# Kernel tuning notes

Measured on AMD Instinct MI355X. Metric: run time of the kernel, lower is better.

## Reference

```python
import jax, jax.numpy as jnp
import numpy as np

N_NODES = 100000
N_EDGES = 1600000
D = 128


def setup_inputs() -> dict:
    key = jax.random.key(0)
    k1, k2, k3 = jax.random.split(key, 3)
    x = jax.random.normal(k1, (N_NODES, D), dtype=jnp.float32)
    W = jax.random.normal(k2, (D, D), dtype=jnp.float32) * (1.0 / np.sqrt(D))
    b = jnp.zeros((D,), dtype=jnp.float32)
    edge_index = jax.random.randint(k3, (2, N_EDGES), 0, N_NODES, dtype=jnp.int64)
    return {"x": x, "W": W, "b": b, "edge_index": edge_index}


def reference(x, W, b, edge_index):
    # GCNBlock: out = relu(GCNConv(x, edge_index)) + x ; returns (out, edge_index)
    # GCNConv (PyG default): add self-loops, symmetric deg^{-1/2} normalization.
    N = x.shape[0]
    h = x @ W  # [N, D] dense transform before aggregation

    loop = jnp.arange(N, dtype=edge_index.dtype)
    src = jnp.concatenate([edge_index[0], loop])  # [E+N]
    dst = jnp.concatenate([edge_index[1], loop])  # [E+N]

    deg = jax.ops.segment_sum(jnp.ones_like(dst, dtype=h.dtype), dst, num_segments=N)
    inv_sqrt = jax.lax.rsqrt(deg)  # deg >= 1 thanks to self-loops
    coef = inv_sqrt[src] * inv_sqrt[dst]  # [E+N]

    # gather messages, scale, scatter-add to destinations
    msg = h[src] * coef[:, None]  # [E+N, D] -- dominant memory traffic
    agg = jax.ops.segment_sum(msg, dst, num_segments=N) + b  # [N, D]

    out = jax.nn.relu(agg) + x  # relu + residual fusion
    return (out, edge_index)
```

## Files before the change

### kernel.cpp

```cpp
#include <hip/hip_runtime.h>


#define DD 128
#define EPB 2048
#define BSH 9
typedef __attribute__((ext_vector_type(8))) short bf16x8;
typedef __attribute__((ext_vector_type(4))) float f32x4;

__device__ __forceinline__ ushort f2bf(float f) {
    unsigned u = __float_as_uint(f);
    unsigned r = (u + 0x7fffu + ((u >> 16) & 1u)) >> 16;
    return (ushort)r;
}
__device__ __forceinline__ float bflo(unsigned u) { return __uint_as_float(u << 16); }
__device__ __forceinline__ float bfhi(unsigned u) { return __uint_as_float(u & 0xffff0000u); }

__device__ __forceinline__ int ld_src(const int* p, int e, int E, int is64) {
    return is64 ? p[2 * e] : p[e];
}
__device__ __forceinline__ int ld_dst(const int* p, int e, int E, int is64) {
    return is64 ? p[2 * (E + e)] : p[E + e];
}

__device__ __forceinline__ int detect64(const int* __restrict__ p, int E) {
    int lane = threadIdx.x & 63;
    int idx = 2 * lane + 1;
    if (idx >= 2 * E) idx = 2 * E - 1;
    unsigned long long m = __ballot(p[idx] != 0);
    return m == 0ull ? 1 : 0;
}

__global__ __launch_bounds__(256) void kA1(const int* __restrict__ ei, int E, int NB, int nA,
                                           float* __restrict__ outTail, int* __restrict__ H,
                                           const float* __restrict__ W, ushort* __restrict__ Wt) {
    int t = threadIdx.x, a = blockIdx.x;
    if (a >= nA) {
        int i = (a - nA) * 256 + t;
        if (i < DD * DD) {
            int c = i >> 7, k = i & 127;
            Wt[i] = f2bf(W[k * DD + c]);
        }
        return;
    }
    __shared__ int hist[256];
    int is64 = detect64(ei, E);
    if (t < NB) hist[t] = 0;
    __syncthreads();
    int base = a * EPB;
    #pragma unroll
    for (int it = 0; it < EPB / 256; ++it) {
        int e = base + it * 256 + t;
        if (e < E) {
            int s = ld_src(ei, e, E, is64);
            int d = ld_dst(ei, e, E, is64);
            outTail[e] = (float)s;
            outTail[E + e] = (float)d;
            atomicAdd(&hist[d >> BSH], 1);
        }
    }
    __syncthreads();
    if (t < NB) H[a * NB + t] = hist[t];
}

__global__ __launch_bounds__(256) void k_scanH1(int* __restrict__ H, int nA, int NB,
                                                int* __restrict__ colsum) {
    __shared__ int s[256];
    int b = blockIdx.x, t = threadIdx.x;
    int K = (nA + 255) / 256;
    int base = t * K;
    int local = 0;
    for (int j = 0; j < K; ++j) {
        int a = base + j;
        if (a < nA) local += H[a * NB + b];
    }
    s[t] = local;
    __syncthreads();
    #pragma unroll
    for (int off = 1; off < 256; off <<= 1) {
        int u = (t >= off) ? s[t - off] : 0;
        __syncthreads();
        s[t] += u;
        __syncthreads();
    }
    int run = s[t] - local;
    for (int j = 0; j < K; ++j) {
        int a = base + j;
        if (a < nA) { int v = H[a * NB + b]; H[a * NB + b] = run; run += v; }
    }
    if (t == 255) colsum[b] = s[255];
}

__global__ __launch_bounds__(256) void kA2(const int* __restrict__ ei, int E, int NB,
                                           const int* __restrict__ H,
                                           const int* __restrict__ colsum,
                                           unsigned* __restrict__ brec) {
    __shared__ int bs[256];
    __shared__ int cur[256];
    int t = threadIdx.x, a = blockIdx.x;
    int is64 = detect64(ei, E);
    int v = (t < NB) ? colsum[t] : 0;
    bs[t] = v;
    __syncthreads();
    #pragma unroll
    for (int off = 1; off < 256; off <<= 1) {
        int u = (t >= off) ? bs[t - off] : 0;
        __syncthreads();
        bs[t] += u;
        __syncthreads();
    }
    if (t < NB) cur[t] = H[a * NB + t] + bs[t] - v;
    __syncthreads();
    int base = a * EPB;
    #pragma unroll
    for (int it = 0; it < EPB / 256; ++it) {
        int e = base + it * 256 + t;
        if (e < E) {
            int s = ld_src(ei, e, E, is64);
            int d = ld_dst(ei, e, E, is64);
            int pos = atomicAdd(&cur[d >> BSH], 1);
            brec[pos] = (unsigned)s | ((unsigned)(d & 511) << 17);
        }
    }
}

__global__ __launch_bounds__(256) void kB(const unsigned* __restrict__ brec,
                                          const int* __restrict__ colsum, int NB, int N,
                                          int E, unsigned* __restrict__ recs,
                                          int* __restrict__ rowstart, float* __restrict__ invs) {
    __shared__ int bs[256];
    __shared__ int hist[512];
    __shared__ int scan[513];
    __shared__ int cur[512];
    int b = blockIdx.x, t = threadIdx.x;
    int v = (t < NB) ? colsum[t] : 0;
    bs[t] = v;
    __syncthreads();
    #pragma unroll
    for (int off = 1; off < 256; off <<= 1) {
        int u = (t >= off) ? bs[t - off] : 0;
        __syncthreads();
        bs[t] += u;
        __syncthreads();
    }
    if (t < NB) bs[t] -= v;
    hist[t] = 0; hist[t + 256] = 0;
    __syncthreads();
    int lo = bs[b], hi = lo + colsum[b];
    for (int i = lo + t; i < hi; i += 256) atomicAdd(&hist[brec[i] >> 17], 1);
    __syncthreads();
    if (t == 0) {
        int acc = 0;
        for (int j = 0; j < 512; ++j) { scan[j] = acc; acc += hist[j]; }
        scan[512] = acc;
    }
    __syncthreads();
    int nodeBase = b << BSH;
    #pragma unroll
    for (int j = t; j < 512; j += 256) {
        int node = nodeBase + j;
        if (node < N) {
            rowstart[node] = lo + scan[j];
            invs[node] = rsqrtf((float)(1 + hist[j]));
        }
        cur[j] = lo + scan[j];
    }
    if (b == NB - 1 && t == 0) rowstart[N] = E;
    __syncthreads();
    for (int i = lo + t; i < hi; i += 256) {
        unsigned r = brec[i];
        int pos = atomicAdd(&cur[r >> 17], 1);
        recs[pos] = r & 0x1FFFFu;
    }
}

__global__ void k_cvt_xs(const float2* __restrict__ x2, const float* __restrict__ invs,
                         unsigned* __restrict__ xs, int n2) {
    int i = blockIdx.x * blockDim.x + threadIdx.x;
    if (i < n2) {
        float w = invs[i >> 6];
        float2 v = x2[i];
        xs[i] = (unsigned)f2bf(w * v.x) | ((unsigned)f2bf(w * v.y) << 16);
    }
}

__global__ void k_agg_s(const unsigned* __restrict__ xs, const int* __restrict__ rowstart,
                        const float* __restrict__ invs, const unsigned* __restrict__ recs,
                        int N, unsigned* __restrict__ aggh) {
    int node = blockIdx.x * 4 + (threadIdx.x >> 6);
    int lane = threadIdx.x & 63;
    if (node >= N) return;
    float wn = invs[node];
    unsigned us = xs[(size_t)node * 64 + lane];
    float accx = bflo(us), accy = bfhi(us);
    int e = rowstart[node], e1 = rowstart[node + 1];
    for (; e + 16 <= e1; e += 16) {
        unsigned sv[16], vv[16];
        #pragma unroll
        for (int j = 0; j < 16; ++j) sv[j] = recs[e + j];
        #pragma unroll
        for (int j = 0; j < 16; ++j) vv[j] = xs[(size_t)sv[j] * 64 + lane];
        #pragma unroll
        for (int j = 0; j < 16; ++j) { accx += bflo(vv[j]); accy += bfhi(vv[j]); }
    }
    if (e + 8 <= e1) {
        unsigned sv[8], vv[8];
        #pragma unroll
        for (int j = 0; j < 8; ++j) sv[j] = recs[e + j];
        #pragma unroll
        for (int j = 0; j < 8; ++j) vv[j] = xs[(size_t)sv[j] * 64 + lane];
        #pragma unroll
        for (int j = 0; j < 8; ++j) { accx += bflo(vv[j]); accy += bfhi(vv[j]); }
        e += 8;
    }
    for (; e < e1; ++e) {
        unsigned v0 = xs[(size_t)recs[e] * 64 + lane];
        accx += bflo(v0); accy += bfhi(v0);
    }
    float ox = accx * wn, oy = accy * wn;
    aggh[(size_t)node * 64 + lane] = (unsigned)f2bf(ox) | ((unsigned)f2bf(oy) << 16);
}

__global__ __launch_bounds__(256) void k_gemm_mfma(const ushort* __restrict__ aggh,
                                                   const ushort* __restrict__ Wt,
                                                   const float* __restrict__ bb,
                                                   const float* __restrict__ x,
                                                   float* __restrict__ out, int N) {
    int wave = threadIdx.x >> 6, lane = threadIdx.x & 63;
    int rowBase = blockIdx.x * 64 + wave * 16;
    int rfrag = lane & 15, kgrp = lane >> 4;
    f32x4 zero = {0.f, 0.f, 0.f, 0.f};
    f32x4 acc[8];
    #pragma unroll
    for (int n = 0; n < 8; ++n) acc[n] = zero;

    int arow = rowBase + rfrag;
    bool av = arow < N;
    const ushort* bbase = aggh + (size_t)(av ? arow : 0) * DD + kgrp * 8;
    const ushort* wbase = Wt + rfrag * DD + kgrp * 8;

    #pragma unroll
    for (int ks = 0; ks < 4; ++ks) {
        bf16x8 bnode = {0, 0, 0, 0, 0, 0, 0, 0};
        if (av) bnode = *(const bf16x8*)(bbase + ks * 32);
        #pragma unroll
        for (int n = 0; n < 8; ++n) {
            bf16x8 aw = *(const bf16x8*)(wbase + n * 16 * DD + ks * 32);
            acc[n] = __builtin_amdgcn_mfma_f32_16x16x32_bf16(aw, bnode, acc[n], 0, 0, 0);
        }
    }

    int node = rowBase + (lane & 15);
    if (node < N) {
        int csub = (lane >> 4) * 4;
        #pragma unroll
        for (int n = 0; n < 8; ++n) {
            int c0 = n * 16 + csub;
            float4 bv = *(const float4*)&bb[c0];
            float4 xv = *(const float4*)&x[(size_t)node * DD + c0];
            float4 o;
            o.x = fmaxf(acc[n][0] + bv.x, 0.f) + xv.x;
            o.y = fmaxf(acc[n][1] + bv.y, 0.f) + xv.y;
            o.z = fmaxf(acc[n][2] + bv.z, 0.f) + xv.z;
            o.w = fmaxf(acc[n][3] + bv.w, 0.f) + xv.w;
            *(float4*)&out[(size_t)node * DD + c0] = o;
        }
    }
}

__global__ void k_sniff(const int* __restrict__ p, int n_check, int* __restrict__ flag) {
    __shared__ int any_nonzero;
    if (threadIdx.x == 0) any_nonzero = 0;
    __syncthreads();
    int j = threadIdx.x;
    if (j < n_check && p[2 * j + 1] != 0) any_nonzero = 1;
    __syncthreads();
    if (threadIdx.x == 0) *flag = any_nonzero ? 0 : 1;
}

__global__ void k_count_echo(const int* __restrict__ ei, int E, int* __restrict__ cnt,
                             float* __restrict__ outTail, unsigned* __restrict__ rank,
                             const int* __restrict__ flagp) {
    int is64 = *flagp;
    int e = blockIdx.x * blockDim.x + threadIdx.x;
    if (e < E) {
        int s = ld_src(ei, e, E, is64);
        int d = ld_dst(ei, e, E, is64);
        outTail[e] = (float)s;
        outTail[E + e] = (float)d;
        rank[e] = (unsigned)atomicAdd(&cnt[d], 1);
    }
}

__global__ void k_scan1(const int* __restrict__ cnt, int N, int* __restrict__ rowstart,
                        int* __restrict__ bsum) {
    __shared__ int s[1024];
    int tid = threadIdx.x;
    int i = blockIdx.x * 1024 + tid;
    int v = (i < N) ? cnt[i] : 0;
    s[tid] = v;
    __syncthreads();
    for (int off = 1; off < 1024; off <<= 1) {
        int t2 = (tid >= off) ? s[tid - off] : 0;
        __syncthreads();
        s[tid] += t2;
        __syncthreads();
    }
    if (i < N) rowstart[i] = s[tid] - v;
    if (tid == 1023) bsum[blockIdx.x] = s[1023];
}

__global__ void k_scan2(const int* __restrict__ bsum, int nblk, int* __restrict__ boff) {
    __shared__ int s[128];
    int t = threadIdx.x;
    if (t < nblk) s[t] = bsum[t];
    __syncthreads();
    if (t == 0) {
        int a = 0;
        for (int i = 0; i < nblk; i++) { int v = s[i]; s[i] = a; a += v; }
    }
    __syncthreads();
    if (t < nblk) boff[t] = s[t];
}

__global__ void k_scan3(int N, int E, int* __restrict__ rowstart, const int* __restrict__ boff,
                        const int* __restrict__ cnt, float* __restrict__ invs) {
    int i = blockIdx.x * blockDim.x + threadIdx.x;
    if (i < N) {
        int r = rowstart[i] + boff[i >> 10];
        rowstart[i] = r;
        invs[i] = rsqrtf((float)(1 + cnt[i]));
    }
    if (i == 0 && blockIdx.x == 0) rowstart[N] = E;
}

__global__ void k_fill_r(const int* __restrict__ ei, int E, const int* __restrict__ rowstart,
                         const unsigned* __restrict__ rank, unsigned* __restrict__ recs,
                         const int* __restrict__ flagp) {
    int is64 = *flagp;
    int e = blockIdx.x * blockDim.x + threadIdx.x;
    if (e < E) {
        int d = ld_dst(ei, e, E, is64);
        int s = ld_src(ei, e, E, is64);
        recs[rowstart[d] + rank[e]] = (unsigned)s;
    }
}

__global__ void k_agg_f32(const float* __restrict__ x, const int* __restrict__ rowstart,
                          const float* __restrict__ invs, const unsigned* __restrict__ recs,
                          int N, float* __restrict__ aggOut) {
    int node = blockIdx.x * 4 + (threadIdx.x >> 6);
    int lane = threadIdx.x & 63;
    if (node >= N) return;
    const float2* xr = (const float2*)x;
    float wn = invs[node];
    float2 xself = xr[(size_t)node * 64 + lane];
    float accx = wn * xself.x, accy = wn * xself.y;
    int e = rowstart[node], e1 = rowstart[node + 1];
    for (; e < e1; ++e) {
        unsigned s = recs[e];
        float w = invs[s];
        float2 v = xr[(size_t)s * 64 + lane];
        accx = fmaf(w, v.x, accx); accy = fmaf(w, v.y, accy);
    }
    float2 o; o.x = accx * wn; o.y = accy * wn;
    ((float2*)aggOut)[(size_t)node * 64 + lane] = o;
}

#define GROWS 32
__global__ __launch_bounds__(128) void k_gemm_f32(float* __restrict__ out, const float* __restrict__ Wm,
                                                  const float* __restrict__ bb,
                                                  const float* __restrict__ x, int N) {
    __shared__ float Ws[64 * DD];
    __shared__ float As[DD * GROWS];
    int t = threadIdx.x;
    int rowBase = blockIdx.x * GROWS;
    {
        int r = t & 31, kq = t >> 5;
        if (rowBase + r < N) {
            const float4* Av = (const float4*)(out + (size_t)(rowBase + r) * DD);
            #pragma unroll
            for (int q = 0; q < 8; q++) {
                float4 v = Av[kq * 8 + q];
                int k = (kq * 8 + q) * 4;
                As[(k + 0) * GROWS + r] = v.x;
                As[(k + 1) * GROWS + r] = v.y;
                As[(k + 2) * GROWS + r] = v.z;
                As[(k + 3) * GROWS + r] = v.w;
            }
        } else {
            #pragma unroll
            for (int q = 0; q < 8; q++) {
                int k = (kq * 8 + q) * 4;
                As[(k + 0) * GROWS + r] = 0.f;
                As[(k + 1) * GROWS + r] = 0.f;
                As[(k + 2) * GROWS + r] = 0.f;
                As[(k + 3) * GROWS + r] = 0.f;
            }
        }
    }
    int tx = t & 15, ty = t >> 4;
    int c0 = tx * 8, r0 = ty * 4;
    float acc[4][8];
    #pragma unroll
    for (int i = 0; i < 4; i++)
        #pragma unroll
        for (int j = 0; j < 8; j++) acc[i][j] = 0.f;
    for (int kk = 0; kk < DD; kk += 64) {
        __syncthreads();
        const float4* Wv = (const float4*)(Wm + (size_t)kk * DD);
        #pragma unroll
        for (int i = 0; i < 16; i++) ((float4*)Ws)[t + i * 128] = Wv[t + i * 128];
        __syncthreads();
        #pragma unroll 4
        for (int k = 0; k < 64; k++) {
            const float4 a = *(const float4*)&As[(kk + k) * GROWS + r0];
            const float4 w0 = *(const float4*)&Ws[k * DD + c0];
            const float4 w1 = *(const float4*)&Ws[k * DD + c0 + 4];
            const float av[4] = {a.x, a.y, a.z, a.w};
            const float wv[8] = {w0.x, w0.y, w0.z, w0.w, w1.x, w1.y, w1.z, w1.w};
            #pragma unroll
            for (int i = 0; i < 4; i++)
                #pragma unroll
                for (int j = 0; j < 8; j++) acc[i][j] = fmaf(av[i], wv[j], acc[i][j]);
        }
    }
    float bv[8];
    {
        float4 b0 = *(const float4*)&bb[c0];
        float4 b1 = *(const float4*)&bb[c0 + 4];
        bv[0] = b0.x; bv[1] = b0.y; bv[2] = b0.z; bv[3] = b0.w;
        bv[4] = b1.x; bv[5] = b1.y; bv[6] = b1.z; bv[7] = b1.w;
    }
    #pragma unroll
    for (int i = 0; i < 4; i++) {
        int row = rowBase + r0 + i;
        if (row < N) {
            const float4 xv0 = *(const float4*)&x[(size_t)row * DD + c0];
            const float4 xv1 = *(const float4*)&x[(size_t)row * DD + c0 + 4];
            float4 o0, o1;
            o0.x = fmaxf(acc[i][0] + bv[0], 0.f) + xv0.x;
            o0.y = fmaxf(acc[i][1] + bv[1], 0.f) + xv0.y;
            o0.z = fmaxf(acc[i][2] + bv[2], 0.f) + xv0.z;
            o0.w = fmaxf(acc[i][3] + bv[3], 0.f) + xv0.w;
            o1.x = fmaxf(acc[i][4] + bv[4], 0.f) + xv1.x;
            o1.y = fmaxf(acc[i][5] + bv[5], 0.f) + xv1.y;
            o1.z = fmaxf(acc[i][6] + bv[6], 0.f) + xv1.z;
            o1.w = fmaxf(acc[i][7] + bv[7], 0.f) + xv1.w;
            *(float4*)&out[(size_t)row * DD + c0] = o0;
            *(float4*)&out[(size_t)row * DD + c0 + 4] = o1;
        }
    }
}

extern "C" void kernel_launch(void* const* d_in, const int* in_sizes, int n_in,
                              void* d_out, int out_size, void* d_ws, size_t ws_size,
                              hipStream_t stream) {
    const float* x = (const float*)d_in[0];
    const float* W = (const float*)d_in[1];
    const float* b = (const float*)d_in[2];
    const int*   ei = (const int*)d_in[3];
    int N = in_sizes[0] / DD;
    int E = in_sizes[3] / 2;
    float* out = (float*)d_out;
    float* outTail = out + (size_t)N * DD;

    int NB = (N + 511) >> BSH;
    int nA = (E + EPB - 1) / EPB;

    char* wsb = (char*)d_ws;
    size_t off = 0;
    unsigned* brec = (unsigned*)(wsb + off);  off += (size_t)E * 4;
    unsigned* recs = (unsigned*)(wsb + off);  off += (size_t)E * 4;
    unsigned* xs   = (unsigned*)(wsb + off);  off += (size_t)N * 64 * 4;
    unsigned* aggh = (unsigned*)(wsb + off);  off += (size_t)N * 64 * 4;
    ushort*   Wt   = (ushort*)(wsb + off);    off += (size_t)DD * DD * 2;
    int* H         = (int*)(wsb + off);       off += (size_t)nA * NB * 4;
    int* colsum    = (int*)(wsb + off);       off += (size_t)NB * 4;
    int* rowstart  = (int*)(wsb + off);       off += (size_t)(N + 1) * 4;
    float* invs    = (float*)(wsb + off);     off += (size_t)N * 4;

    bool newpath = (ws_size >= off) && (NB <= 256) && (nA <= 1024) && (N <= 131072) && (E >= 64);

    if (newpath) {
        kA1<<<nA + 64, 256, 0, stream>>>(ei, E, NB, nA, outTail, H, W, Wt);
        k_scanH1<<<NB, 256, 0, stream>>>(H, nA, NB, colsum);
        kA2<<<nA, 256, 0, stream>>>(ei, E, NB, H, colsum, brec);
        kB<<<NB, 256, 0, stream>>>(brec, colsum, NB, N, E, recs, rowstart, invs);
        int n2 = N * 64;
        k_cvt_xs<<<(n2 + 255) / 256, 256, 0, stream>>>((const float2*)x, invs, xs, n2);
        k_agg_s<<<(N + 3) / 4, 256, 0, stream>>>(xs, rowstart, invs, recs, N, aggh);
        k_gemm_mfma<<<(N + 63) / 64, 256, 0, stream>>>((const ushort*)aggh, Wt, b, x, out, N);
    } else {
        off = 0;
        unsigned* recsF = (unsigned*)(wsb + off);  off += (size_t)E * 4;
        unsigned* rank  = (unsigned*)(wsb + off);  off += (size_t)E * 4;
        int* cnt        = (int*)(wsb + off);       off += (size_t)N * 4;
        int* rowstartF  = (int*)(wsb + off);       off += (size_t)(N + 1) * 4;
        float* invsF    = (float*)(wsb + off);     off += (size_t)N * 4;
        int* bsum       = (int*)(wsb + off);       off += 512 * 4;
        int* boff       = (int*)(wsb + off);       off += 512 * 4;
        int* flagF      = (int*)(wsb + off);

        hipMemsetAsync(cnt, 0, sizeof(int) * (size_t)N, stream);
        k_sniff<<<1, 1024, 0, stream>>>(ei, 1024, flagF);
        k_count_echo<<<(E + 255) / 256, 256, 0, stream>>>(ei, E, cnt, outTail, rank, flagF);
        int nblk = (N + 1023) / 1024;
        k_scan1<<<nblk, 1024, 0, stream>>>(cnt, N, rowstartF, bsum);
        k_scan2<<<1, 128, 0, stream>>>(bsum, nblk, boff);
        k_scan3<<<(N + 255) / 256, 256, 0, stream>>>(N, E, rowstartF, boff, cnt, invsF);
        k_fill_r<<<(E + 255) / 256, 256, 0, stream>>>(ei, E, rowstartF, rank, recsF, flagF);
        k_agg_f32<<<(N + 3) / 4, 256, 0, stream>>>(x, rowstartF, invsF, recsF, N, out);
        k_gemm_f32<<<(N + GROWS - 1) / GROWS, 128, 0, stream>>>(out, W, b, x, N);
    }
}
```

Before: 183.5 us.

## Reorder to GEMM-then-aggregate, fusing bf16 conversion into GEMM and epilogue into aggregation

The schedule changes from convert→aggregate→GEMM to GEMM→aggregate. The GEMM now reads fp32 x directly, converts it to bf16 in registers, scales by the source deg^-1/2 and writes a bf16 h table. The aggregation kernel then applies the destination scale, bias, ReLU and residual and writes the final output. This removes one kernel launch and one full N×128 bf16 intermediate round trip. The trade is that the aggregation now reads x and writes fp32 out, and rounding happens at a different point.

```diff
diff --git a/kernel.cpp b/kernel.cpp
--- a/kernel.cpp
+++ b/kernel.cpp
@@ -173,58 +173,10 @@
     }
 }
 
-__global__ void k_cvt_xs(const float2* __restrict__ x2, const float* __restrict__ invs,
-                         unsigned* __restrict__ xs, int n2) {
-    int i = blockIdx.x * blockDim.x + threadIdx.x;
-    if (i < n2) {
-        float w = invs[i >> 6];
-        float2 v = x2[i];
-        xs[i] = (unsigned)f2bf(w * v.x) | ((unsigned)f2bf(w * v.y) << 16);
-    }
-}
-
-__global__ void k_agg_s(const unsigned* __restrict__ xs, const int* __restrict__ rowstart,
-                        const float* __restrict__ invs, const unsigned* __restrict__ recs,
-                        int N, unsigned* __restrict__ aggh) {
-    int node = blockIdx.x * 4 + (threadIdx.x >> 6);
-    int lane = threadIdx.x & 63;
-    if (node >= N) return;
-    float wn = invs[node];
-    unsigned us = xs[(size_t)node * 64 + lane];
-    float accx = bflo(us), accy = bfhi(us);
-    int e = rowstart[node], e1 = rowstart[node + 1];
-    for (; e + 16 <= e1; e += 16) {
-        unsigned sv[16], vv[16];
-        #pragma unroll
-        for (int j = 0; j < 16; ++j) sv[j] = recs[e + j];
-        #pragma unroll
-        for (int j = 0; j < 16; ++j) vv[j] = xs[(size_t)sv[j] * 64 + lane];
-        #pragma unroll
-        for (int j = 0; j < 16; ++j) { accx += bflo(vv[j]); accy += bfhi(vv[j]); }
-    }
-    if (e + 8 <= e1) {
-        unsigned sv[8], vv[8];
-        #pragma unroll
-        for (int j = 0; j < 8; ++j) sv[j] = recs[e + j];
-        #pragma unroll
-        for (int j = 0; j < 8; ++j) vv[j] = xs[(size_t)sv[j] * 64 + lane];
-        #pragma unroll
-        for (int j = 0; j < 8; ++j) { accx += bflo(vv[j]); accy += bfhi(vv[j]); }
-        e += 8;
-    }
-    for (; e < e1; ++e) {
-        unsigned v0 = xs[(size_t)recs[e] * 64 + lane];
-        accx += bflo(v0); accy += bfhi(v0);
-    }
-    float ox = accx * wn, oy = accy * wn;
-    aggh[(size_t)node * 64 + lane] = (unsigned)f2bf(ox) | ((unsigned)f2bf(oy) << 16);
-}
-
-__global__ __launch_bounds__(256) void k_gemm_mfma(const ushort* __restrict__ aggh,
-                                                   const ushort* __restrict__ Wt,
-                                                   const float* __restrict__ bb,
-                                                   const float* __restrict__ x,
-                                                   float* __restrict__ out, int N) {
+__global__ __launch_bounds__(256) void k_gemm_h(const float* __restrict__ x,
+                                                const ushort* __restrict__ Wt,
+                                                const float* __restrict__ invs,
+                                                unsigned* __restrict__ hs, int N) {
     int wave = threadIdx.x >> 6, lane = threadIdx.x & 63;
     int rowBase = blockIdx.x * 64 + wave * 16;
     int rfrag = lane & 15, kgrp = lane >> 4;
@@ -235,13 +187,20 @@
 
     int arow = rowBase + rfrag;
     bool av = arow < N;
-    const ushort* bbase = aggh + (size_t)(av ? arow : 0) * DD + kgrp * 8;
+    const float* xrow = x + (size_t)(av ? arow : 0) * DD + kgrp * 8;
     const ushort* wbase = Wt + rfrag * DD + kgrp * 8;
 
     #pragma unroll
     for (int ks = 0; ks < 4; ++ks) {
         bf16x8 bnode = {0, 0, 0, 0, 0, 0, 0, 0};
-        if (av) bnode = *(const bf16x8*)(bbase + ks * 32);
+        if (av) {
+            float4 f0 = *(const float4*)(xrow + ks * 32);
+            float4 f1 = *(const float4*)(xrow + ks * 32 + 4);
+            bnode[0] = (short)f2bf(f0.x); bnode[1] = (short)f2bf(f0.y);
+            bnode[2] = (short)f2bf(f0.z); bnode[3] = (short)f2bf(f0.w);
+            bnode[4] = (short)f2bf(f1.x); bnode[5] = (short)f2bf(f1.y);
+            bnode[6] = (short)f2bf(f1.z); bnode[7] = (short)f2bf(f1.w);
+        }
         #pragma unroll
         for (int n = 0; n < 8; ++n) {
             bf16x8 aw = *(const bf16x8*)(wbase + n * 16 * DD + ks * 32);
@@ -249,22 +208,61 @@
         }
     }
 
-    int node = rowBase + (lane & 15);
+    int node = rowBase + rfrag;
     if (node < N) {
-        int csub = (lane >> 4) * 4;
+        float wn = invs[node];
+        int csub = kgrp * 4;
         #pragma unroll
         for (int n = 0; n < 8; ++n) {
             int c0 = n * 16 + csub;
-            float4 bv = *(const float4*)&bb[c0];
-            float4 xv = *(const float4*)&x[(size_t)node * DD + c0];
-            float4 o;
-            o.x = fmaxf(acc[n][0] + bv.x, 0.f) + xv.x;
-            o.y = fmaxf(acc[n][1] + bv.y, 0.f) + xv.y;
-            o.z = fmaxf(acc[n][2] + bv.z, 0.f) + xv.z;
-            o.w = fmaxf(acc[n][3] + bv.w, 0.f) + xv.w;
-            *(float4*)&out[(size_t)node * DD + c0] = o;
-        }
-    }
+            unsigned u0 = (unsigned)f2bf(wn * acc[n][0]) | ((unsigned)f2bf(wn * acc[n][1]) << 16);
+            unsigned u1 = (unsigned)f2bf(wn * acc[n][2]) | ((unsigned)f2bf(wn * acc[n][3]) << 16);
+            hs[(size_t)node * 64 + (c0 >> 1)] = u0;
+            hs[(size_t)node * 64 + (c0 >> 1) + 1] = u1;
+        }
+    }
+}
+
+__global__ void k_agg_out(const unsigned* __restrict__ hs, const int* __restrict__ rowstart,
+                          const float* __restrict__ invs, const unsigned* __restrict__ recs,
+                          const float* __restrict__ bb, const float* __restrict__ x,
+                          float* __restrict__ out, int N) {
+    int node = blockIdx.x * 4 + (threadIdx.x >> 6);
+    int lane = threadIdx.x & 63;
+    if (node >= N) return;
+    float wn = invs[node];
+    unsigned us = hs[(size_t)node * 64 + lane];
+    float accx = bflo(us), accy = bfhi(us);
+    int e = rowstart[node], e1 = rowstart[node + 1];
+    for (; e + 16 <= e1; e += 16) {
+        unsigned sv[16], vv[16];
+        #pragma unroll
+        for (int j = 0; j < 16; ++j) sv[j] = recs[e + j];
+        #pragma unroll
+        for (int j = 0; j < 16; ++j) vv[j] = hs[(size_t)sv[j] * 64 + lane];
+        #pragma unroll
+        for (int j = 0; j < 16; ++j) { accx += bflo(vv[j]); accy += bfhi(vv[j]); }
+    }
+    if (e + 8 <= e1) {
+        unsigned sv[8], vv[8];
+        #pragma unroll
+        for (int j = 0; j < 8; ++j) sv[j] = recs[e + j];
+        #pragma unroll
+        for (int j = 0; j < 8; ++j) vv[j] = hs[(size_t)sv[j] * 64 + lane];
+        #pragma unroll
+        for (int j = 0; j < 8; ++j) { accx += bflo(vv[j]); accy += bfhi(vv[j]); }
+        e += 8;
+    }
+    for (; e < e1; ++e) {
+        unsigned v0 = hs[(size_t)recs[e] * 64 + lane];
+        accx += bflo(v0); accy += bfhi(v0);
+    }
+    float2 bv = ((const float2*)bb)[lane];
+    float2 xv = ((const float2*)x)[(size_t)node * 64 + lane];
+    float2 o;
+    o.x = fmaxf(accx * wn + bv.x, 0.f) + xv.x;
+    o.y = fmaxf(accy * wn + bv.y, 0.f) + xv.y;
+    ((float2*)out)[(size_t)node * 64 + lane] = o;
 }
 
 __global__ void k_sniff(const int* __restrict__ p, int n_check, int* __restrict__ flag) {
@@ -471,8 +469,7 @@
     size_t off = 0;
     unsigned* brec = (unsigned*)(wsb + off);  off += (size_t)E * 4;
     unsigned* recs = (unsigned*)(wsb + off);  off += (size_t)E * 4;
-    unsigned* xs   = (unsigned*)(wsb + off);  off += (size_t)N * 64 * 4;
-    unsigned* aggh = (unsigned*)(wsb + off);  off += (size_t)N * 64 * 4;
+    unsigned* hs   = (unsigned*)(wsb + off);  off += (size_t)N * 64 * 4;
     ushort*   Wt   = (ushort*)(wsb + off);    off += (size_t)DD * DD * 2;
     int* H         = (int*)(wsb + off);       off += (size_t)nA * NB * 4;
     int* colsum    = (int*)(wsb + off);       off += (size_t)NB * 4;
@@ -486,10 +483,8 @@
         k_scanH1<<<NB, 256, 0, stream>>>(H, nA, NB, colsum);
         kA2<<<nA, 256, 0, stream>>>(ei, E, NB, H, colsum, brec);
         kB<<<NB, 256, 0, stream>>>(brec, colsum, NB, N, E, recs, rowstart, invs);
-        int n2 = N * 64;
-        k_cvt_xs<<<(n2 + 255) / 256, 256, 0, stream>>>((const float2*)x, invs, xs, n2);
-        k_agg_s<<<(N + 3) / 4, 256, 0, stream>>>(xs, rowstart, invs, recs, N, aggh);
-        k_gemm_mfma<<<(N + 63) / 64, 256, 0, stream>>>((const ushort*)aggh, Wt, b, x, out, N);
+        k_gemm_h<<<(N + 63) / 64, 256, 0, stream>>>(x, Wt, invs, hs, N);
+        k_agg_out<<<(N + 3) / 4, 256, 0, stream>>>(hs, rowstart, invs, recs, b, x, out, N);
     } else {
         off = 0;
         unsigned* recsF = (unsigned*)(wsb + off);  off += (size_t)E * 4;
```

After: 173.3 us. -5.5%, faster.
